# Kernel optimization log

Measured on AMD Instinct MI355X. Metric: run time of the kernel, lower is better.

The kernel has to match this reference:

```python
import jax, jax.numpy as jnp
import numpy as np

N_EMBD = 1024
N_HEAD = 16
B, L = 2, 2048


def setup_inputs() -> dict:
    key = jax.random.key(0)
    k1, k2, k3, k4 = jax.random.split(key, 4)
    x = jax.random.normal(k1, (B, L, N_EMBD), dtype=jnp.float32)
    W_qkv = jax.random.normal(k2, (N_EMBD, 3 * N_EMBD), dtype=jnp.float32) * 0.02
    b_qkv = jnp.zeros((3 * N_EMBD,), dtype=jnp.float32)
    W_o = jax.random.normal(k3, (N_EMBD, N_EMBD), dtype=jnp.float32) * 0.02
    b_o = jnp.zeros((N_EMBD,), dtype=jnp.float32)
    mask_len = jax.random.randint(k4, (B,), 1, L, dtype=jnp.int32)
    return {"x": x, "W_qkv": W_qkv, "b_qkv": b_qkv, "W_o": W_o, "b_o": b_o,
            "mask_len": mask_len}


def reference(x, W_qkv, b_qkv, W_o, b_o, mask_len):
    Bx, Lx, E = x.shape
    H = N_HEAD
    D = E // H
    # causal mask [1,1,L,L]; then zero out query rows i >= mask_len[b]
    mask = jnp.tri(Lx)[None, None, :, :]
    row_invalid = jnp.arange(Lx).reshape(1, 1, Lx, 1) >= mask_len.reshape(Bx, 1, 1, 1)
    mask = jnp.where(row_invalid, 0.0, mask)  # [B,1,L,L]
    # QKV projection; note original packs per-head 3D-chunks: reshape (B,L,H,3D)
    h = x @ W_qkv + b_qkv                      # [B,L,3E]
    h = h.reshape(Bx, Lx, H, 3 * D).transpose(0, 2, 1, 3)  # [B,H,L,3D]
    q, k, v = jnp.split(h, 3, axis=-1)         # each [B,H,L,D]
    attn = jnp.einsum('bhqd,bhkd->bhqk', q, k) / jnp.sqrt(jnp.float32(D))
    attn = jnp.where(mask == 0, -1e18, attn)
    attn = jax.nn.softmax(attn, axis=-1)
    # dropout: deterministic (train=False) -> identity
    y = jnp.einsum('bhqk,bhkd->bhqd', attn, v)  # [B,H,L,D]
    y = y.transpose(0, 2, 1, 3).reshape(Bx, Lx, E)
    return y @ W_o + b_o
```

## Files before the change

kernel.cpp:

```cpp
#include <hip/hip_runtime.h>

typedef unsigned short u16;
typedef unsigned int u32;
typedef __bf16 bf16x8 __attribute__((ext_vector_type(8)));
typedef float f32x4 __attribute__((ext_vector_type(4)));
typedef u16 u16x4 __attribute__((ext_vector_type(4)));
typedef u16 u16x8 __attribute__((ext_vector_type(8)));

#define LSEQ 2048
#define EMB  1024
#define NH   16
#define HDIM 64

#define QSCALE 0.1803368808f

#if __has_builtin(__builtin_amdgcn_exp2f)
#define EXP2(x) __builtin_amdgcn_exp2f(x)
#else
#define EXP2(x) __expf((x) * 0.6931471805599453f)
#endif

__device__ __forceinline__ u16 cvt_bf(float f) {
  __bf16 h = (__bf16)f;
  return __builtin_bit_cast(u16, h);
}
__device__ __forceinline__ float bf2f(u16 v) {
  return __uint_as_float(((unsigned)v) << 16);
}
__device__ __forceinline__ void async16(void* lds, const void* g) {
  __builtin_amdgcn_global_load_lds((const __attribute__((address_space(1))) void*)g,
                                   (__attribute__((address_space(3))) void*)lds, 16, 0, 0);
}
__device__ __forceinline__ f32x4 mfma16(bf16x8 a, bf16x8 b, f32x4 c) {
  return __builtin_amdgcn_mfma_f32_16x16x32_bf16(a, b, c, 0, 0, 0);
}

__global__ void prep(const float* __restrict__ x, u16* __restrict__ xb,
                     const float* __restrict__ Wqkv, u16* __restrict__ WqkvT,
                     const float* __restrict__ Wo, u16* __restrict__ WoT) {
  __shared__ float tile[32][33];
  const int bid = blockIdx.x;
  const int tid = threadIdx.x;
  if (bid < 2048) {
    const int n4 = 1024 * 1024;
    for (int i = bid * 256 + tid; i < n4; i += 2048 * 256) {
      float4 v = ((const float4*)x)[i];
      u16x4 o = { cvt_bf(v.x), cvt_bf(v.y), cvt_bf(v.z), cvt_bf(v.w) };
      ((u16x4*)xb)[i] = o;
    }
    return;
  }
  const int idx = bid - 2048;
  const int bx = idx & 127, by = idx >> 7;
  const int Kd = 1024;
  const float* in;
  u16* out;
  int Nd, n0;
  if (bx < 96) { in = Wqkv; out = WqkvT; Nd = 3072; n0 = bx * 32; }
  else         { in = Wo;   out = WoT;   Nd = 1024; n0 = (bx - 96) * 32; }
  const int k0 = by * 32;
  const int tx = tid & 31, ty = tid >> 5;
#pragma unroll
  for (int i = 0; i < 4; ++i)
    tile[ty + i * 8][tx] = in[(size_t)(k0 + ty + i * 8) * Nd + n0 + tx];
  __syncthreads();
#pragma unroll
  for (int i = 0; i < 4; ++i)
    out[(size_t)(n0 + ty + i * 8) * Kd + k0 + tx] = cvt_bf(tile[tx][ty + i * 8]);
}

template<int NCOLS, int MODE, int BM>
__launch_bounds__(256)
__global__ void gemm_bt(const u16* __restrict__ A, const u16* __restrict__ Bt,
                        const float* __restrict__ bias, float* __restrict__ Out,
                        u16* __restrict__ Qo, u16* __restrict__ Ko, u16* __restrict__ Vo) {
  constexpr int MF = BM / 32;
  constexpr int ABUF = BM * 32;
  __shared__ __attribute__((aligned(16))) u16 SMEM[3 * ABUF + 3 * 128 * 32];
  u16* As = SMEM;
  u16* Bs = SMEM + 3 * ABUF;
  const int tid = threadIdx.x;
  const int w = tid >> 6, l = tid & 63;
  const int g = l >> 4, cc = l & 15;
  constexpr int GX = NCOLS / 128;
  constexpr int NWG = (4096 / BM) * GX;
  constexpr int CPX = NWG / 8;
  const int orig = blockIdx.y * GX + blockIdx.x;
  const int wgid = (orig & 7) * CPX + (orig >> 3);
  const int m0 = (wgid / GX) * BM, n0 = (wgid % GX) * 128;
  const int wm = w >> 1, wn = w & 1;
  const int K = 1024;
  const int srow = tid >> 2;
  const int scol = (tid & 3) * 8;
  const u16* Ag = A + (size_t)(m0 + srow) * K + scol;
  const u16* Bg = Bt + (size_t)(n0 + srow) * K + scol;
  f32x4 acc[MF][4] = {};

  auto stage = [&](int buf, int k0) {
    async16(&As[buf * ABUF + w * 512], Ag + k0);
    if constexpr (BM == 128)
      async16(&As[buf * ABUF + 2048 + w * 512], Ag + (size_t)64 * K + k0);
    async16(&Bs[buf * 4096 + w * 512], Bg + k0);
    async16(&Bs[buf * 4096 + 2048 + w * 512], Bg + (size_t)64 * K + k0);
  };

  stage(0, 0);
  stage(1, 32);
  int buf = 0;
  for (int k0 = 0; k0 < K; k0 += 32) {
    if (k0 + 32 < K) {
      if constexpr (BM == 128) asm volatile("s_waitcnt vmcnt(4)" ::: "memory");
      else                     asm volatile("s_waitcnt vmcnt(3)" ::: "memory");
    } else {
      asm volatile("s_waitcnt vmcnt(0)" ::: "memory");
    }
    __builtin_amdgcn_s_barrier();
    __builtin_amdgcn_sched_barrier(0);
    if (k0 + 64 < K) {
      int nb = buf + 2; if (nb >= 3) nb -= 3;
      stage(nb, k0 + 64);
    }
    bf16x8 af[MF], bfr[4];
#pragma unroll
    for (int mf = 0; mf < MF; ++mf)
      af[mf] = *(const bf16x8*)&As[buf * ABUF + (wm * (BM / 2) + mf * 16 + cc) * 32 + g * 8];
#pragma unroll
    for (int nf = 0; nf < 4; ++nf)
      bfr[nf] = *(const bf16x8*)&Bs[buf * 4096 + (wn * 64 + nf * 16 + cc) * 32 + g * 8];
#pragma unroll
    for (int mf = 0; mf < MF; ++mf)
#pragma unroll
      for (int nf = 0; nf < 4; ++nf)
        acc[mf][nf] = mfma16(af[mf], bfr[nf], acc[mf][nf]);
    if (++buf == 3) buf = 0;
  }

  if constexpr (MODE == 0) {
    __syncthreads();
    char* pane0 = (char*)SMEM;
    char* pane1 = (char*)(SMEM + 3 * ABUF);
    const int bb = m0 >> 11;
    {
      const int nbase = n0 + wn * 64;
      const int hd = nbase / 192, rem = nbase - hd * 192, which = rem >> 6;
      char* P = wn ? pane1 : pane0;
#pragma unroll
      for (int mf = 0; mf < MF; ++mf) {
#pragma unroll
        for (int nf = 0; nf < 4; ++nf) {
          int d = nf * 16 + cc;
          float bv = bias[nbase + d];
#pragma unroll
          for (int r = 0; r < 4; ++r) {
            int ml = wm * 64 + mf * 16 + g * 4 + r;
            float val = acc[mf][nf][r] + bv;
            if (which == 0) val *= QSCALE;
            u16 h = cvt_bf(val);
            if (which == 2) *(u16*)(P + d * 272 + ml * 2) = h;
            else            *(u16*)(P + ml * 144 + d * 2) = h;
          }
        }
      }
    }
    __syncthreads();
#pragma unroll
    for (int wi = 0; wi < 2; ++wi) {
      const int nb = n0 + wi * 64;
      const int hd = nb / 192, rem = nb - hd * 192, wh = rem >> 6;
      const int bh = bb * NH + hd;
      const int ls0 = m0 & (LSEQ - 1);
      char* P = wi ? pane1 : pane0;
      if (wh == 2) {
        u16* dstb = Vo + (size_t)bh * HDIM * LSEQ + ls0;
#pragma unroll
        for (int it = 0; it < 4; ++it) {
          int idx = it * 256 + tid;
          int row = idx >> 4;
          int colB = (idx & 15) * 16;
          int4 v = *(const int4*)(P + row * 272 + colB);
          *(int4*)((char*)(dstb + (size_t)row * LSEQ) + colB) = v;
        }
      } else {
        u16* dst = (wh == 0 ? Qo : Ko) + ((size_t)bh * LSEQ + ls0) * HDIM;
#pragma unroll
        for (int it = 0; it < 4; ++it) {
          int idx = it * 256 + tid;
          int row = idx >> 3;
          int colB = (idx & 7) * 16;
          int4 v = *(const int4*)(P + row * 144 + colB);
          *(int4*)((char*)dst + row * 128 + colB) = v;
        }
      }
    }
  } else {
#pragma unroll
    for (int mf = 0; mf < MF; ++mf) {
#pragma unroll
      for (int nf = 0; nf < 4; ++nf) {
        int n = n0 + wn * 64 + nf * 16 + cc;
        float bv = bias[n];
#pragma unroll
        for (int r = 0; r < 4; ++r) {
          int m = m0 + wm * (BM / 2) + mf * 16 + g * 4 + r;
          Out[(size_t)m * NCOLS + n] = acc[mf][nf][r] + bv;
        }
      }
    }
  }
}

__launch_bounds__(256)
__global__ void attn_fwd(const u16* __restrict__ Q, const u16* __restrict__ Kb,
                         const u16* __restrict__ Vt, const int* __restrict__ mask_len,
                         u16* __restrict__ Y) {
  __shared__ __attribute__((aligned(16))) u16 Ks[2][64 * 64];
  __shared__ __attribute__((aligned(16))) u16 Vs[2][64 * 64];
  __shared__ __attribute__((aligned(16))) u16 Ps[4 * 16 * 64];
  const int tid = threadIdx.x;
  const int i = blockIdx.x;

  if (i >= 1024) {
    float* partial = (float*)Ks;
    u16* mv = (u16*)((char*)Ks + 1024);
    int bh = i - 1024, b = bh >> 4, h = bh & (NH - 1);
    int d = tid >> 2, part = tid & 3;
    const u16* src = Vt + ((size_t)bh * HDIM + d) * LSEQ + part * 512;
    float s = 0.f;
    for (int ii = 0; ii < 512; ii += 8) {
      u16x8 v = *(const u16x8*)&src[ii];
#pragma unroll
      for (int jj = 0; jj < 8; ++jj) s += bf2f(v[jj]);
    }
    partial[tid] = s;
    __syncthreads();
    if (part == 0) {
      float t = partial[tid] + partial[tid + 1] + partial[tid + 2] + partial[tid + 3];
      mv[d] = cvt_bf(t * (1.0f / (float)LSEQ));
    }
    __syncthreads();
    int lo = mask_len[b];
    if (lo < 0) lo = 0;
    if (lo > LSEQ) lo = LSEQ;
    int total = (LSEQ - lo) * HDIM;
    for (int idx = tid; idx < total; idx += 256) {
      int row = lo + (idx >> 6), dd = idx & 63;
      Y[((size_t)b * LSEQ + row) * EMB + h * HDIM + dd] = mv[dd];
    }
    return;
  }

  const int w = tid >> 6, l = tid & 63;
  const int g = l >> 4, cc = l & 15;
  const int bh = i & 31;
  const int k = i >> 5, grp = k >> 3, j = k & 7;
  int qblk;
  if (grp == 0) qblk = 31 - j;
  else if (grp == 1) qblk = j;
  else if (grp == 2) qblk = 23 - j;
  else qblk = 8 + j;
  const int q0 = qblk * 64;
  const int nt = qblk + 1;
  const int b = bh >> 4, h = bh & (NH - 1);

  const int lo = mask_len[b];
  if (q0 >= lo) return;

  const int sr = w * 8 + (l >> 3);
  const int pb = (l & 7) * 16;
  char* Pw = (char*)&Ps[w * 16 * 64];
  const int xc = (cc & 7) << 4;

  auto stageKV = [&](int buf, int t) {
    const int kv0 = t * 64;
#pragma unroll
    for (int ch = 0; ch < 2; ++ch) {
      int R = sr + ch * 32;
      int dcol = (pb ^ ((R & 7) << 4)) >> 1;
      async16((char*)Ks[buf] + ch * 4096 + w * 1024,
              Kb + ((size_t)bh * LSEQ + kv0 + R) * HDIM + dcol);
      async16((char*)Vs[buf] + ch * 4096 + w * 1024,
              Vt + ((size_t)bh * HDIM + R) * LSEQ + kv0 + dcol);
    }
  };

  const u16* Qg = Q + ((size_t)bh * LSEQ + q0 + w * 16) * HDIM;
  bf16x8 qf0 = *(const bf16x8*)&Qg[cc * HDIM + g * 8];
  bf16x8 qf1 = *(const bf16x8*)&Qg[cc * HDIM + 32 + g * 8];

  bf16x8 onesf;
#pragma unroll
  for (int z = 0; z < 8; ++z) onesf[z] = (__bf16)1.0f;

  f32x4 o[4] = {};
  f32x4 ls = {};

  stageKV(0, 0);

  for (int t = 0; t < nt; ++t) {
    const int cur = t & 1;
    if (t + 1 < nt) {
      stageKV(cur ^ 1, t + 1);
      asm volatile("s_waitcnt vmcnt(4)" ::: "memory");
    } else {
      asm volatile("s_waitcnt vmcnt(0)" ::: "memory");
    }
    __builtin_amdgcn_s_barrier();
    __builtin_amdgcn_sched_barrier(0);
    const char* KsB = (const char*)Ks[cur];
    const char* VsB = (const char*)Vs[cur];

    f32x4 sf[4] = {};
    __builtin_amdgcn_s_setprio(1);
#pragma unroll
    for (int nf = 0; nf < 4; ++nf) {
      bf16x8 kf0 = *(const bf16x8*)(KsB + (nf * 16 + cc) * 128 + ((g * 16) ^ xc));
      bf16x8 kf1 = *(const bf16x8*)(KsB + (nf * 16 + cc) * 128 + ((64 + g * 16) ^ xc));
      sf[nf] = mfma16(qf0, kf0, sf[nf]);
      sf[nf] = mfma16(qf1, kf1, sf[nf]);
    }
    __builtin_amdgcn_s_setprio(0);

    if (t == nt - 1) {
#pragma unroll
      for (int nf = 0; nf < 4; ++nf) {
        int kvl = nf * 16 + cc;
#pragma unroll
        for (int r = 0; r < 4; ++r)
          if (kvl > w * 16 + g * 4 + r) sf[nf][r] = -1e30f;
      }
    }

#pragma unroll
    for (int r = 0; r < 4; ++r) {
      int q = g * 4 + r;
      int xr = (q & 7) << 4;
#pragma unroll
      for (int nf = 0; nf < 4; ++nf) {
        float pv = EXP2(sf[nf][r]);
        *(u16*)(Pw + q * 128 + (((nf * 16 + cc) * 2) ^ xr)) = cvt_bf(pv);
      }
    }
    asm volatile("s_waitcnt lgkmcnt(0)" ::: "memory");
    __builtin_amdgcn_sched_barrier(0);

    bf16x8 pf0 = *(const bf16x8*)(Pw + cc * 128 + ((g * 16) ^ xc));
    bf16x8 pf1 = *(const bf16x8*)(Pw + cc * 128 + ((64 + g * 16) ^ xc));
    __builtin_amdgcn_s_setprio(1);
    ls = mfma16(pf1, onesf, mfma16(pf0, onesf, ls));
#pragma unroll
    for (int nf = 0; nf < 4; ++nf) {
      bf16x8 vf0 = *(const bf16x8*)(VsB + (nf * 16 + cc) * 128 + ((g * 16) ^ xc));
      bf16x8 vf1 = *(const bf16x8*)(VsB + (nf * 16 + cc) * 128 + ((64 + g * 16) ^ xc));
      o[nf] = mfma16(pf0, vf0, o[nf]);
      o[nf] = mfma16(pf1, vf1, o[nf]);
    }
    __builtin_amdgcn_s_setprio(0);
    __builtin_amdgcn_s_barrier();
  }

#pragma unroll
  for (int r = 0; r < 4; ++r) {
    int row = q0 + w * 16 + g * 4 + r;
    if (row < lo) {
      float inv = 1.0f / ls[r];
      size_t base = ((size_t)b * LSEQ + row) * EMB + h * HDIM;
#pragma unroll
      for (int nf = 0; nf < 4; ++nf)
        Y[base + nf * 16 + cc] = cvt_bf(o[nf][r] * inv);
    }
  }
}

extern "C" void kernel_launch(void* const* d_in, const int* in_sizes, int n_in,
                              void* d_out, int out_size, void* d_ws, size_t ws_size,
                              hipStream_t stream) {
  (void)in_sizes; (void)n_in; (void)out_size; (void)ws_size;
  const float* x    = (const float*)d_in[0];
  const float* Wqkv = (const float*)d_in[1];
  const float* bqkv = (const float*)d_in[2];
  const float* Wo   = (const float*)d_in[3];
  const float* bo   = (const float*)d_in[4];
  const int* mask_len = (const int*)d_in[5];
  float* out = (float*)d_out;

  u16* ws = (u16*)d_ws;
  u16* xb    = ws;
  u16* wqkvt = ws + (size_t)4 * 1024 * 1024;
  u16* wot   = wqkvt + (size_t)3 * 1024 * 1024;
  u16* Qb    = wot + (size_t)1024 * 1024;
  u16* Kb    = Qb + (size_t)4 * 1024 * 1024;
  u16* Vtb   = Kb + (size_t)4 * 1024 * 1024;
  u16* Yb    = xb;

  prep<<<6144, 256, 0, stream>>>(x, xb, Wqkv, wqkvt, Wo, wot);
  gemm_bt<3072, 0, 128><<<dim3(24, 32), 256, 0, stream>>>(xb, wqkvt, bqkv, nullptr, Qb, Kb, Vtb);
  attn_fwd<<<1056, 256, 0, stream>>>(Qb, Kb, Vtb, mask_len, Yb);
  gemm_bt<1024, 1, 64><<<dim3(8, 64), 256, 0, stream>>>(Yb, wot, bo, out, nullptr, nullptr, nullptr);
}
```

Baseline: 98.17 us.

## Regroup QKV GEMM tiles by Q/K/V type, skip masked-row Q/K tiles, swizzle LDS

The QKV projection's column tiles are remapped so each workgroup computes the same projection type (Q, K or V) for two heads, using two separate B-row base pointers. Q and K tiles whose query rows all lie beyond mask_len return early, on the assumption that attention never reads those rows. The epilogue staging buffers switch from padded strides to XOR-swizzled layouts to avoid LDS bank conflicts. The early exit leaves Q/K rows unwritten, so correctness depends on the attention kernel skipping invalid rows.

```diff
diff --git a/kernel.cpp b/kernel.cpp
--- a/kernel.cpp
+++ b/kernel.cpp
@@ -73,7 +73,8 @@
 __launch_bounds__(256)
 __global__ void gemm_bt(const u16* __restrict__ A, const u16* __restrict__ Bt,
                         const float* __restrict__ bias, float* __restrict__ Out,
-                        u16* __restrict__ Qo, u16* __restrict__ Ko, u16* __restrict__ Vo) {
+                        u16* __restrict__ Qo, u16* __restrict__ Ko, u16* __restrict__ Vo,
+                        const int* __restrict__ mask_len) {
   constexpr int MF = BM / 32;
   constexpr int ABUF = BM * 32;
   __shared__ __attribute__((aligned(16))) u16 SMEM[3 * ABUF + 3 * 128 * 32];
@@ -90,18 +91,35 @@
   const int m0 = (wgid / GX) * BM, n0 = (wgid % GX) * 128;
   const int wm = w >> 1, wn = w & 1;
   const int K = 1024;
+
+  int type = 0, tbh = 0;
+  if constexpr (MODE == 0) {
+    const int tb = wgid % GX;
+    type = tb >> 3;
+    tbh = tb & 7;
+    const int bb = m0 >> 11;
+    if (type < 2 && (m0 & (LSEQ - 1)) >= mask_len[bb]) return;
+  }
+
   const int srow = tid >> 2;
   const int scol = (tid & 3) * 8;
   const u16* Ag = A + (size_t)(m0 + srow) * K + scol;
-  const u16* Bg = Bt + (size_t)(n0 + srow) * K + scol;
+  const u16 *Bg0, *Bg1;
+  if constexpr (MODE == 0) {
+    Bg0 = Bt + (size_t)((2 * tbh) * 192 + type * 64 + srow) * K + scol;
+    Bg1 = Bt + (size_t)((2 * tbh + 1) * 192 + type * 64 + srow) * K + scol;
+  } else {
+    Bg0 = Bt + (size_t)(n0 + srow) * K + scol;
+    Bg1 = Bt + (size_t)(n0 + srow + 64) * K + scol;
+  }
   f32x4 acc[MF][4] = {};
 
   auto stage = [&](int buf, int k0) {
     async16(&As[buf * ABUF + w * 512], Ag + k0);
     if constexpr (BM == 128)
       async16(&As[buf * ABUF + 2048 + w * 512], Ag + (size_t)64 * K + k0);
-    async16(&Bs[buf * 4096 + w * 512], Bg + k0);
-    async16(&Bs[buf * 4096 + 2048 + w * 512], Bg + (size_t)64 * K + k0);
+    async16(&Bs[buf * 4096 + w * 512], Bg0 + k0);
+    async16(&Bs[buf * 4096 + 2048 + w * 512], Bg1 + k0);
   };
 
   stage(0, 0);
@@ -141,23 +159,27 @@
     char* pane1 = (char*)(SMEM + 3 * ABUF);
     const int bb = m0 >> 11;
     {
-      const int nbase = n0 + wn * 64;
-      const int hd = nbase / 192, rem = nbase - hd * 192, which = rem >> 6;
+      const int hw = 2 * tbh + wn;
+      const float* bptr = bias + hw * 192 + type * 64;
       char* P = wn ? pane1 : pane0;
 #pragma unroll
       for (int mf = 0; mf < MF; ++mf) {
 #pragma unroll
         for (int nf = 0; nf < 4; ++nf) {
           int d = nf * 16 + cc;
-          float bv = bias[nbase + d];
+          float bv = bptr[d];
 #pragma unroll
           for (int r = 0; r < 4; ++r) {
             int ml = wm * 64 + mf * 16 + g * 4 + r;
             float val = acc[mf][nf][r] + bv;
-            if (which == 0) val *= QSCALE;
+            if (type == 0) val *= QSCALE;
             u16 h = cvt_bf(val);
-            if (which == 2) *(u16*)(P + d * 272 + ml * 2) = h;
-            else            *(u16*)(P + ml * 144 + d * 2) = h;
+            if (type == 2) {
+              int off = (ml * 2) & 127;
+              *(u16*)(P + d * 256 + ((ml & 64) << 1) + (off ^ ((d & 7) << 4))) = h;
+            } else {
+              *(u16*)(P + ml * 128 + ((d * 2) ^ ((ml & 7) << 4))) = h;
+            }
           }
         }
       }
@@ -165,29 +187,28 @@
     __syncthreads();
 #pragma unroll
     for (int wi = 0; wi < 2; ++wi) {
-      const int nb = n0 + wi * 64;
-      const int hd = nb / 192, rem = nb - hd * 192, wh = rem >> 6;
-      const int bh = bb * NH + hd;
+      const int head = 2 * tbh + wi;
+      const int bh = bb * NH + head;
       const int ls0 = m0 & (LSEQ - 1);
       char* P = wi ? pane1 : pane0;
-      if (wh == 2) {
+      if (type == 2) {
         u16* dstb = Vo + (size_t)bh * HDIM * LSEQ + ls0;
 #pragma unroll
         for (int it = 0; it < 4; ++it) {
           int idx = it * 256 + tid;
           int row = idx >> 4;
           int colB = (idx & 15) * 16;
-          int4 v = *(const int4*)(P + row * 272 + colB);
+          int4 v = *(const int4*)(P + row * 256 + (colB & 128) + ((colB & 112) ^ ((row & 7) << 4)));
           *(int4*)((char*)(dstb + (size_t)row * LSEQ) + colB) = v;
         }
       } else {
-        u16* dst = (wh == 0 ? Qo : Ko) + ((size_t)bh * LSEQ + ls0) * HDIM;
+        u16* dst = (type == 0 ? Qo : Ko) + ((size_t)bh * LSEQ + ls0) * HDIM;
 #pragma unroll
         for (int it = 0; it < 4; ++it) {
           int idx = it * 256 + tid;
           int row = idx >> 3;
           int colB = (idx & 7) * 16;
-          int4 v = *(const int4*)(P + row * 144 + colB);
+          int4 v = *(const int4*)(P + row * 128 + (colB ^ ((row & 7) << 4)));
           *(int4*)((char*)dst + row * 128 + colB) = v;
         }
       }
@@ -393,7 +414,7 @@
   u16* Yb    = xb;
 
   prep<<<6144, 256, 0, stream>>>(x, xb, Wqkv, wqkvt, Wo, wot);
-  gemm_bt<3072, 0, 128><<<dim3(24, 32), 256, 0, stream>>>(xb, wqkvt, bqkv, nullptr, Qb, Kb, Vtb);
+  gemm_bt<3072, 0, 128><<<dim3(24, 32), 256, 0, stream>>>(xb, wqkvt, bqkv, nullptr, Qb, Kb, Vtb, mask_len);
   attn_fwd<<<1056, 256, 0, stream>>>(Qb, Kb, Vtb, mask_len, Yb);
-  gemm_bt<1024, 1, 64><<<dim3(8, 64), 256, 0, stream>>>(Yb, wot, bo, out, nullptr, nullptr, nullptr);
-}
+  gemm_bt<1024, 1, 64><<<dim3(8, 64), 256, 0, stream>>>(Yb, wot, bo, out, nullptr, nullptr, nullptr, nullptr);
+}
```

Measured after the change: 98.97 us. No clear change (+0.8%).
